# Performance work log

Measured on AMD Instinct MI355X. Metric: run time of the kernel, lower is better.

## Reference

```python
import jax, jax.numpy as jnp
from jax import lax
import numpy as np

HIDDEN = 1024
FEAT = 512
PREV = 10
PRED = 20
BATCH = 1024


def setup_inputs() -> dict:
    key = jax.random.key(0)
    ks = jax.random.split(key, 12)
    s_in = 1.0 / np.sqrt(FEAT)
    s_h = 1.0 / np.sqrt(HIDDEN)
    return {
        "real_input": jax.random.normal(ks[0], (BATCH, PREV + PRED, FEAT), jnp.float32),
        "fake_input": jax.random.normal(ks[1], (BATCH, PRED, FEAT), jnp.float32),
        "Wx": jax.random.normal(ks[2], (FEAT, 4 * HIDDEN), jnp.float32) * s_in,
        "Wh": jax.random.normal(ks[3], (HIDDEN, 4 * HIDDEN), jnp.float32) * s_h,
        "b": jnp.zeros((4 * HIDDEN,), jnp.float32),
        "w2": jax.random.normal(ks[4], (HIDDEN, 1), jnp.float32) * s_h,
        "b2": jnp.zeros((1,), jnp.float32),
        "w3": jax.random.normal(ks[5], (1, 1), jnp.float32),
        "b3": jnp.zeros((1,), jnp.float32),
        "w4": jax.random.normal(ks[6], (1, 1), jnp.float32),
        "b4": jnp.zeros((1,), jnp.float32),
    }


def _lstm_hidden_states(seq, Wx, Wh, b):
    # seq: [B, T, F] -> hidden states hs: [T, B, H]
    B = seq.shape[0]
    xz = jnp.einsum("btf,fk->btk", seq, Wx) + b  # precompute input projections

    def step(carry, xz_t):
        h, c = carry
        z = xz_t + h @ Wh  # [B, 4H]
        i, f, g, o = jnp.split(z, 4, axis=-1)
        i = jax.nn.sigmoid(i)
        f = jax.nn.sigmoid(f)
        g = jnp.tanh(g)
        o = jax.nn.sigmoid(o)
        c = f * c + i * g
        h = o * jnp.tanh(c)
        return (h, c), h

    h0 = jnp.zeros((B, Wh.shape[0]), seq.dtype)
    _, hs = lax.scan(step, (h0, h0), jnp.swapaxes(xz, 0, 1))
    return hs


def _dense_chain(h, w2, b2, w3, b3, w4, b4):
    x = jnp.tanh(h @ w2 + b2)
    x = jnp.tanh(x @ w3 + b3)
    x = jnp.tanh(x @ w4 + b4)
    return x


def reference(real_input, fake_input, Wx, Wh, b, w2, b2, w3, b3, w4, b4):
    # trajectory_real[k] is the prefix real_input[:, :PREV+k+1]; running the
    # LSTM from zero state over each prefix equals taking hidden state at
    # step PREV+k of a single scan over the full sequence.
    fake_seq = jnp.concatenate([real_input[:, :PREV, :], fake_input], axis=1)

    hs_real = _lstm_hidden_states(real_input, Wx, Wh, b)[PREV:PREV + PRED]  # [PRED,B,H]
    hs_fake = _lstm_hidden_states(fake_seq, Wx, Wh, b)[PREV:PREV + PRED]

    real_pred = _dense_chain(hs_real, w2, b2, w3, b3, w4, b4)  # [PRED,B,1]
    fake_pred = _dense_chain(hs_fake, w2, b2, w3, b3, w4, b4)

    real_pred = jnp.swapaxes(real_pred, 0, 1)  # [B,PRED,1]
    fake_pred = jnp.swapaxes(fake_pred, 0, 1)
    return real_pred, fake_pred
```

## Files before the change

kernel.cpp:

```cpp
#include <hip/hip_runtime.h>
#include <hip/hip_bf16.h>
#include <stdint.h>
#include <string.h>

#define HIDDEN 1024
#define FEAT   512
#define PREV   10
#define PRED   20
#define BATCH  1024
#define KTOT   (HIDDEN + FEAT)
#define N4H    4096
#define TSTEPS (PREV + PRED)
#define NBLK   512
#define NTHR   512

typedef __attribute__((ext_vector_type(8))) short short8;
typedef __attribute__((ext_vector_type(4))) float f32x4;
typedef unsigned long long ull;

typedef __attribute__((address_space(3))) unsigned int u32_lds;
typedef const __attribute__((address_space(1))) unsigned int u32_gbl;

__device__ __forceinline__ void async16(void* lds, const void* g) {
  u32_lds* lp = (u32_lds*)(unsigned int)(uintptr_t)lds;
  u32_gbl* gp = (u32_gbl*)(uintptr_t)g;
  __builtin_amdgcn_global_load_lds(gp, lp, 16, 0, 0);
}

__device__ __forceinline__ float sigmoidf_(float x) {
  return 1.0f / (1.0f + __expf(-x));
}
__device__ __forceinline__ float tanhf_(float x) {
  return 1.0f - 2.0f / (1.0f + __expf(2.0f * x));
}

__device__ __forceinline__ ull cload(const void* p) {
  return __hip_atomic_load((const ull*)p, __ATOMIC_RELAXED, __HIP_MEMORY_SCOPE_AGENT);
}
__device__ __forceinline__ void cstore(void* p, ull v) {
  __hip_atomic_store((ull*)p, v, __ATOMIC_RELAXED, __HIP_MEMORY_SCOPE_AGENT);
}

__global__ void pack_w_kernel(const float* __restrict__ Wx, const float* __restrict__ Wh,
                              __hip_bfloat16* __restrict__ WpT) {
  __shared__ float tile[64][65];
  const int k0 = blockIdx.x * 64, n0 = blockIdx.y * 64;
  const int tid = threadIdx.x;
  const float* src = (k0 < HIDDEN) ? (Wh + (size_t)k0 * N4H) : (Wx + (size_t)(k0 - HIDDEN) * N4H);
  {
    const int jl = tid & 15, g = (tid >> 4) & 3, klb = tid >> 6;
#pragma unroll
    for (int it = 0; it < 16; ++it) {
      int kl = klb + it * 4;
      tile[kl][4 * jl + g] = src[(size_t)kl * N4H + g * HIDDEN + (n0 >> 2) + jl];
    }
  }
  __syncthreads();
  {
    const int kl = tid & 63, nlb = tid >> 6;
#pragma unroll
    for (int it = 0; it < 16; ++it) {
      int nl = nlb + it * 4;
      WpT[(size_t)(n0 + nl) * KTOT + k0 + kl] = __float2bfloat16(tile[kl][nl]);
    }
  }
}

__global__ void pack_bias_kernel(const float* __restrict__ b, float* __restrict__ bp) {
  int n = blockIdx.x * 256 + threadIdx.x;
  if (n < N4H) bp[n] = b[(n & 3) * HIDDEN + (n >> 2)];
}

__global__ void cvt_x_kernel(const float* __restrict__ xr, const float* __restrict__ xf,
                             __hip_bfloat16* __restrict__ xrb, __hip_bfloat16* __restrict__ xfb) {
  const int NR4 = BATCH * TSTEPS * FEAT / 4;
  const int NF4 = BATCH * PRED * FEAT / 4;
  int i = blockIdx.x * 256 + threadIdx.x;
  float4 v;
  __hip_bfloat16* dst;
  if (i < NR4) {
    v = ((const float4*)xr)[i];
    dst = xrb + (size_t)i * 4;
  } else {
    int j = i - NR4;
    if (j >= NF4) return;
    v = ((const float4*)xf)[j];
    dst = xfb + (size_t)j * 4;
  }
  dst[0] = __float2bfloat16(v.x);
  dst[1] = __float2bfloat16(v.y);
  dst[2] = __float2bfloat16(v.z);
  dst[3] = __float2bfloat16(v.w);
}

__global__ __launch_bounds__(512, 4)
void lstm_persistent(const __hip_bfloat16* __restrict__ xrb,
                     const __hip_bfloat16* __restrict__ xfb,
                     const __hip_bfloat16* __restrict__ WpT,
                     const float* __restrict__ biasp,
                     const float* __restrict__ w2,
                     __hip_bfloat16* __restrict__ hb0,
                     __hip_bfloat16* __restrict__ hb1,
                     float* __restrict__ cbuf,
                     float* __restrict__ accout,
                     unsigned* __restrict__ bar) {
  __shared__ __align__(16) char smem[40960];
  char* smA = smem;
  char* smB = smem + 8192;

  const int tid = threadIdx.x;
  const int bid = blockIdx.x;
  const int nt = bid & 15, rt = bid >> 4;
  const int n0 = nt * 256;
  const int r0 = rt * 64;
  const int w = tid >> 6, l = tid & 63;
  const int sub = l >> 3;
  const int csrc = (l & 7) ^ sub;
  const int quad = l >> 4, lrow = l & 15;
  const int wm = w & 1, wn = w >> 1;
  const int row_e = tid >> 3, jq = tid & 7;
  unsigned* cnt = bar;
  unsigned* flag = bar + 32;

  const unsigned short* wp_us = (const unsigned short*)WpT;
  float creg[8] = {0.f, 0.f, 0.f, 0.f, 0.f, 0.f, 0.f, 0.f};

#pragma unroll 1
  for (int t = 0; t < TSTEPS; ++t) {
    const unsigned short* hcur = (const unsigned short*)((t & 1) ? hb1 : hb0);
    unsigned short* hnext = (unsigned short*)((t & 1) ? hb0 : hb1);
    const bool active = (t >= PREV) || (rt < 16);

    if (active) {
      if (t == PREV && r0 >= BATCH) {
#pragma unroll
        for (int h2 = 0; h2 < 2; ++h2) {
          size_t base = (size_t)(r0 - BATCH + row_e) * HIDDEN + nt * 64 + h2 * 32 + jq * 4;
          ull d0 = cload(&cbuf[base]);
          ull d1 = cload(&cbuf[base + 2]);
          float2 f0 = *(float2*)&d0, f1 = *(float2*)&d1;
          creg[h2 * 4 + 0] = f0.x;
          creg[h2 * 4 + 1] = f0.y;
          creg[h2 * 4 + 2] = f1.x;
          creg[h2 * 4 + 3] = f1.y;
        }
      }
      const int r0h = (t == PREV && r0 >= BATCH) ? (r0 - BATCH) : r0;

      f32x4 acc[2][4];
#pragma unroll
      for (int a = 0; a < 2; ++a)
#pragma unroll
        for (int b_ = 0; b_ < 4; ++b_) acc[a][b_] = (f32x4){0.f, 0.f, 0.f, 0.f};

#pragma unroll 1
      for (int kt = 0; kt < KTOT / 64; ++kt) {
        const int k0 = kt * 64;
        const unsigned short* bb = wp_us + (size_t)n0 * KTOT + k0;
#pragma unroll
        for (int it = 0; it < 4; ++it)
          async16(smB + (w * 32 + it * 8) * 128,
                  bb + (size_t)(w * 32 + it * 8 + sub) * KTOT + csrc * 8);
        if (k0 < HIDDEN) {
          const unsigned short* ap = hcur + (size_t)(r0h + w * 8 + sub) * HIDDEN + k0 + csrc * 8;
          ull d0 = cload(ap);
          ull d1 = cload(ap + 4);
          ull* lw = (ull*)(smA + (w * 8 + sub) * 128 + (l & 7) * 16);
          lw[0] = d0;
          lw[1] = d1;
        } else {
          const unsigned short* xb;
          size_t xstr;
          if (r0 < BATCH) {
            xb = (const unsigned short*)xrb + ((size_t)r0 * TSTEPS + t) * FEAT + (k0 - HIDDEN);
            xstr = TSTEPS * FEAT;
          } else {
            xb = (const unsigned short*)xfb + ((size_t)(r0 - BATCH) * PRED + (t - PREV)) * FEAT + (k0 - HIDDEN);
            xstr = PRED * FEAT;
          }
          async16(smA + (w * 8) * 128, xb + (size_t)(w * 8 + sub) * xstr + csrc * 8);
        }
        __syncthreads();
#pragma unroll
        for (int kk = 0; kk < 2; ++kk) {
          const int swz = (((kk << 2) + quad) ^ (lrow & 7)) * 16;
          short8 af[2], bf[4];
#pragma unroll
          for (int mi = 0; mi < 2; ++mi)
            af[mi] = *(const short8*)(smA + (wm * 32 + mi * 16 + lrow) * 128 + swz);
#pragma unroll
          for (int ni = 0; ni < 4; ++ni)
            bf[ni] = *(const short8*)(smB + (wn * 64 + ni * 16 + lrow) * 128 + swz);
#pragma unroll
          for (int mi = 0; mi < 2; ++mi)
#pragma unroll
            for (int ni = 0; ni < 4; ++ni)
              acc[mi][ni] = __builtin_amdgcn_mfma_f32_16x16x32_bf16(af[mi], bf[ni], acc[mi][ni], 0, 0, 0);
        }
        __syncthreads();
      }

      float* zb = (float*)smem;
      const int kout = t - PREV;
#pragma unroll 1
      for (int h2 = 0; h2 < 2; ++h2) {
        if ((wn >> 1) == h2) {
          const int cb = (wn & 1) * 64;
#pragma unroll
          for (int mi = 0; mi < 2; ++mi)
#pragma unroll
            for (int ni = 0; ni < 4; ++ni) {
              f32x4 v = acc[mi][ni];
              int col = cb + ni * 16 + lrow;
              int rb = wm * 32 + mi * 16 + quad * 4;
#pragma unroll
              for (int r = 0; r < 4; ++r) zb[(rb + r) * 132 + col] = v[r];
            }
        }
        __syncthreads();
        unsigned short hs[4];
        float cn[4];
        float psum = 0.f;
#pragma unroll
        for (int it = 0; it < 4; ++it) {
          int jloc = jq * 4 + it;
          float4 z4 = *(float4*)&zb[row_e * 132 + jloc * 4];
          float4 bi = *(const float4*)&biasp[n0 + h2 * 128 + jloc * 4];
          int jg = nt * 64 + h2 * 32 + jloc;
          float gi = sigmoidf_(z4.x + bi.x);
          float gf = sigmoidf_(z4.y + bi.y);
          float gg = tanhf_(z4.z + bi.z);
          float go = sigmoidf_(z4.w + bi.w);
          int ci = h2 * 4 + it;
          float cnew = gf * creg[ci] + gi * gg;
          float hnew = go * tanhf_(cnew);
          creg[ci] = cnew;
          cn[it] = cnew;
          __hip_bfloat16 hbv = __float2bfloat16(hnew);
          hs[it] = *(unsigned short*)&hbv;
          if (t >= PREV) psum += hnew * w2[jg];
        }
        const int rg = r0 + row_e;
        const int jg0 = nt * 64 + h2 * 32 + jq * 4;
        ull hpack;
        memcpy(&hpack, hs, 8);
        cstore(&hnext[(size_t)rg * HIDDEN + jg0], hpack);
        if (t == PREV - 1) {
          ull c01, c23;
          memcpy(&c01, &cn[0], 8);
          memcpy(&c23, &cn[2], 8);
          cstore(&cbuf[(size_t)rg * HIDDEN + jg0], c01);
          cstore(&cbuf[(size_t)rg * HIDDEN + jg0 + 2], c23);
        }
        if (t >= PREV) {
          psum += __shfl_down(psum, 4, 8);
          psum += __shfl_down(psum, 2, 8);
          psum += __shfl_down(psum, 1, 8);
          if ((tid & 7) == 0) atomicAdd(&accout[rg * PRED + kout], psum);
        }
        __syncthreads();
      }
    }

    if (t < TSTEPS - 1) {
      __syncthreads();
      if (tid == 0) {
        unsigned ph = (unsigned)(t + 1);
        unsigned old = __hip_atomic_fetch_add(cnt, 1u, __ATOMIC_RELAXED, __HIP_MEMORY_SCOPE_AGENT);
        if (old == NBLK - 1) {
          __hip_atomic_store(cnt, 0u, __ATOMIC_RELAXED, __HIP_MEMORY_SCOPE_AGENT);
          __hip_atomic_store(flag, ph, __ATOMIC_RELAXED, __HIP_MEMORY_SCOPE_AGENT);
        } else {
          while (__hip_atomic_load(flag, __ATOMIC_RELAXED, __HIP_MEMORY_SCOPE_AGENT) < ph)
            __builtin_amdgcn_s_sleep(4);
        }
      }
      __syncthreads();
    }
  }
}

__global__ void final_kernel(const float* __restrict__ accout, const float* __restrict__ b2,
                             const float* __restrict__ w3, const float* __restrict__ b3,
                             const float* __restrict__ w4, const float* __restrict__ b4,
                             float* __restrict__ out) {
  int i = blockIdx.x * 256 + threadIdx.x;
  const int half = BATCH * PRED;
  if (i >= 2 * half) return;
  int r, k;
  if (i < half) {
    r = i / PRED;
    k = i % PRED;
  } else {
    r = BATCH + (i - half) / PRED;
    k = (i - half) % PRED;
  }
  float x = tanhf_(accout[r * PRED + k] + b2[0]);
  x = tanhf_(x * w3[0] + b3[0]);
  x = tanhf_(x * w4[0] + b4[0]);
  out[i] = x;
}

extern "C" void kernel_launch(void* const* d_in, const int* in_sizes, int n_in,
                              void* d_out, int out_size, void* d_ws, size_t ws_size,
                              hipStream_t stream) {
  const float* real_input = (const float*)d_in[0];
  const float* fake_input = (const float*)d_in[1];
  const float* Wx = (const float*)d_in[2];
  const float* Wh = (const float*)d_in[3];
  const float* b  = (const float*)d_in[4];
  const float* w2 = (const float*)d_in[5];
  const float* b2 = (const float*)d_in[6];
  const float* w3 = (const float*)d_in[7];
  const float* b3 = (const float*)d_in[8];
  const float* w4 = (const float*)d_in[9];
  const float* b4 = (const float*)d_in[10];
  float* out = (float*)d_out;

  char* ws = (char*)d_ws;
  size_t off = 0;
  __hip_bfloat16* WpT = (__hip_bfloat16*)(ws + off);  off += (size_t)N4H * KTOT * 2;
  float* biasp = (float*)(ws + off);                  off += (size_t)N4H * 4;
  __hip_bfloat16* xrb = (__hip_bfloat16*)(ws + off);  off += (size_t)BATCH * TSTEPS * FEAT * 2;
  __hip_bfloat16* xfb = (__hip_bfloat16*)(ws + off);  off += (size_t)BATCH * PRED * FEAT * 2;
  __hip_bfloat16* hb0 = (__hip_bfloat16*)(ws + off);  off += (size_t)2 * BATCH * HIDDEN * 2;
  __hip_bfloat16* hb1 = (__hip_bfloat16*)(ws + off);  off += (size_t)2 * BATCH * HIDDEN * 2;
  float* cbuf = (float*)(ws + off);                   off += (size_t)BATCH * HIDDEN * 4;
  float* accout = (float*)(ws + off);                 off += (size_t)2 * BATCH * PRED * 4;
  unsigned* bar = (unsigned*)(ws + off);              off += 256;

  hipMemsetAsync(hb0, 0, (size_t)2 * BATCH * HIDDEN * 2, stream);
  hipMemsetAsync(accout, 0, (size_t)2 * BATCH * PRED * 4, stream);
  hipMemsetAsync(bar, 0, 256, stream);

  pack_w_kernel<<<dim3(KTOT / 64, N4H / 64), 256, 0, stream>>>(Wx, Wh, WpT);
  pack_bias_kernel<<<N4H / 256, 256, 0, stream>>>(b, biasp);
  {
    int n4 = BATCH * TSTEPS * FEAT / 4 + BATCH * PRED * FEAT / 4;
    cvt_x_kernel<<<(n4 + 255) / 256, 256, 0, stream>>>(real_input, fake_input, xrb, xfb);
  }

  {
    const __hip_bfloat16* a_xrb = xrb;
    const __hip_bfloat16* a_xfb = xfb;
    const __hip_bfloat16* a_WpT = WpT;
    const float* a_biasp = biasp;
    const float* a_w2 = w2;
    __hip_bfloat16* a_hb0 = hb0;
    __hip_bfloat16* a_hb1 = hb1;
    float* a_cbuf = cbuf;
    float* a_acc = accout;
    unsigned* a_bar = bar;
    void* args[10] = {&a_xrb, &a_xfb, &a_WpT, &a_biasp, &a_w2,
                      &a_hb0, &a_hb1, &a_cbuf, &a_acc, &a_bar};
    hipError_t e = hipLaunchCooperativeKernel((const void*)lstm_persistent,
                                              dim3(NBLK), dim3(NTHR), args, 0, stream);
    if (e != hipSuccess) {
      lstm_persistent<<<dim3(NBLK), dim3(NTHR), 0, stream>>>(
          xrb, xfb, WpT, biasp, w2, hb0, hb1, cbuf, accout, bar);
    }
  }

  final_kernel<<<(2 * BATCH * PRED + 255) / 256, 256, 0, stream>>>(accout, b2, w3, b3, w4, b4, out);
}
```

Baseline: 1.307 ms.

## Retile LSTM step with double-buffered LDS and phase-specific tile shapes

Splits the per-step GEMM into a templated helper that uses 128-column N tiles (32 tiles) with 64-row M tiles in the shared prefix phase and 128-row M tiles in the two-branch phase, so all 512 blocks stay busy during the first PREV steps instead of half sitting idle. It double-buffers A and B in LDS, prefetching the next K slice (async weight loads, register-staged h loads) while the MFMAs run on the current one. LDS use grows to 64KB per block, which may reduce occupancy, and the extra barriers and changed gate/c-state indexing add complexity.

```diff
diff --git a/kernel.cpp b/kernel.cpp
--- a/kernel.cpp
+++ b/kernel.cpp
@@ -39,6 +39,9 @@
 }
 __device__ __forceinline__ void cstore(void* p, ull v) {
   __hip_atomic_store((ull*)p, v, __ATOMIC_RELAXED, __HIP_MEMORY_SCOPE_AGENT);
+}
+__device__ __forceinline__ void cstore4(void* p, unsigned v) {
+  __hip_atomic_store((unsigned*)p, v, __ATOMIC_RELAXED, __HIP_MEMORY_SCOPE_AGENT);
 }
 
 __global__ void pack_w_kernel(const float* __restrict__ Wx, const float* __restrict__ Wh,
@@ -93,6 +96,179 @@
   dst[3] = __float2bfloat16(v.w);
 }
 
+template <int MT>
+__device__ __forceinline__ void do_step(
+    const unsigned short* __restrict__ hcur, unsigned short* __restrict__ hnext,
+    const unsigned short* __restrict__ xrb, const unsigned short* __restrict__ xfb,
+    const unsigned short* __restrict__ wp_us, const float* __restrict__ biasp,
+    const float* __restrict__ w2, float* __restrict__ cbuf,
+    float* __restrict__ accout, float* __restrict__ creg, char* smem,
+    int t, int r0, int r0a, int nt,
+    int tid, int w, int l, int sub, int csrc, int quad, int lrow) {
+
+  const int n0 = nt * 128;
+  constexpr int NK = KTOT / 64;
+  constexpr int AM = MT / 32;
+  constexpr int AIT = MT / 64;
+  const int wm = w & 1, wn = w >> 1;
+  const int mbase = wm * (MT / 2);
+  const int arow = w * 8 + sub;
+
+  char* sA[2] = {smem, smem + 16384};
+  char* sB[2] = {smem + 32768, smem + 49152};
+
+  f32x4 acc[AM][2];
+#pragma unroll
+  for (int a = 0; a < AM; ++a) {
+    acc[a][0] = (f32x4){0.f, 0.f, 0.f, 0.f};
+    acc[a][1] = (f32x4){0.f, 0.f, 0.f, 0.f};
+  }
+
+  const unsigned short* xbase;
+  size_t xstr;
+  if (r0 < BATCH) {
+    xbase = xrb + ((size_t)r0 * TSTEPS + t) * FEAT;
+    xstr = (size_t)TSTEPS * FEAT;
+  } else {
+    xbase = xfb + ((size_t)(r0 - BATCH) * PRED + (t - PREV)) * FEAT;
+    xstr = (size_t)PRED * FEAT;
+  }
+
+  ull ar[AIT][2];
+
+  {
+    const unsigned short* bb = wp_us + (size_t)n0 * KTOT;
+#pragma unroll
+    for (int it = 0; it < 2; ++it)
+      async16(sB[0] + (it * 64 + w * 8) * 128, bb + (size_t)(it * 64 + arow) * KTOT + csrc * 8);
+#pragma unroll
+    for (int it = 0; it < AIT; ++it) {
+      const unsigned short* ap = hcur + (size_t)(r0a + it * 64 + arow) * HIDDEN + csrc * 8;
+      ar[it][0] = cload(ap);
+      ar[it][1] = cload(ap + 4);
+    }
+  }
+
+#pragma unroll 1
+  for (int kt = 0; kt < NK; ++kt) {
+    const int p = kt & 1, pn = p ^ 1;
+    const int k0 = kt * 64;
+    const bool hk = (k0 < HIDDEN);
+    __syncthreads();
+    if (hk) {
+#pragma unroll
+      for (int it = 0; it < AIT; ++it) {
+        ull* lw = (ull*)(sA[p] + (it * 64 + arow) * 128 + (l & 7) * 16);
+        lw[0] = ar[it][0];
+        lw[1] = ar[it][1];
+      }
+      __syncthreads();
+    }
+    if (kt + 1 < NK) {
+      const int k1 = k0 + 64;
+      const unsigned short* bb = wp_us + (size_t)n0 * KTOT + k1;
+#pragma unroll
+      for (int it = 0; it < 2; ++it)
+        async16(sB[pn] + (it * 64 + w * 8) * 128, bb + (size_t)(it * 64 + arow) * KTOT + csrc * 8);
+      if (k1 < HIDDEN) {
+#pragma unroll
+        for (int it = 0; it < AIT; ++it) {
+          const unsigned short* ap = hcur + (size_t)(r0a + it * 64 + arow) * HIDDEN + k1 + csrc * 8;
+          ar[it][0] = cload(ap);
+          ar[it][1] = cload(ap + 4);
+        }
+      } else {
+#pragma unroll
+        for (int it = 0; it < AIT; ++it)
+          async16(sA[pn] + (it * 64 + w * 8) * 128,
+                  xbase + (size_t)(it * 64 + arow) * xstr + (k1 - HIDDEN) + csrc * 8);
+      }
+    }
+#pragma unroll
+    for (int kk = 0; kk < 2; ++kk) {
+      const int swz = (((kk << 2) + quad) ^ (lrow & 7)) * 16;
+      short8 af[AM], bf[2];
+#pragma unroll
+      for (int mi = 0; mi < AM; ++mi)
+        af[mi] = *(const short8*)(sA[p] + (mbase + mi * 16 + lrow) * 128 + swz);
+#pragma unroll
+      for (int ni = 0; ni < 2; ++ni)
+        bf[ni] = *(const short8*)(sB[p] + (wn * 32 + ni * 16 + lrow) * 128 + swz);
+#pragma unroll
+      for (int mi = 0; mi < AM; ++mi)
+#pragma unroll
+        for (int ni = 0; ni < 2; ++ni)
+          acc[mi][ni] = __builtin_amdgcn_mfma_f32_16x16x32_bf16(af[mi], bf[ni], acc[mi][ni], 0, 0, 0);
+    }
+  }
+  __syncthreads();
+
+  float* zb = (float*)smem;
+  const int kout = t - PREV;
+  constexpr int JT = (MT == 128) ? 4 : 2;
+  const int row_e = (MT == 128) ? (tid >> 2) : (tid >> 3);
+  const int jq = (MT == 128) ? (tid & 3) : (tid & 7);
+#pragma unroll 1
+  for (int h2 = 0; h2 < 2; ++h2) {
+    if ((wn >> 1) == h2) {
+      const int cb = (wn & 1) * 32;
+#pragma unroll
+      for (int mi = 0; mi < AM; ++mi)
+#pragma unroll
+        for (int ni = 0; ni < 2; ++ni) {
+          f32x4 v = acc[mi][ni];
+          const int col = cb + ni * 16 + lrow;
+          const int rb = mbase + mi * 16 + quad * 4;
+#pragma unroll
+          for (int r = 0; r < 4; ++r) zb[(rb + r) * 68 + col] = v[r];
+        }
+    }
+    __syncthreads();
+    unsigned short hs[JT];
+    float cn[JT];
+    float psum = 0.f;
+#pragma unroll
+    for (int it = 0; it < JT; ++it) {
+      const int jloc = jq * JT + it;
+      float4 z4 = *(float4*)&zb[row_e * 68 + jloc * 4];
+      float4 bi = *(const float4*)&biasp[n0 + h2 * 64 + jloc * 4];
+      const int jg = nt * 32 + h2 * 16 + jloc;
+      float gi = sigmoidf_(z4.x + bi.x);
+      float gf = sigmoidf_(z4.y + bi.y);
+      float gg = tanhf_(z4.z + bi.z);
+      float go = sigmoidf_(z4.w + bi.w);
+      const int ci = h2 * JT + it;
+      float cnew = gf * creg[ci] + gi * gg;
+      float hnew = go * tanhf_(cnew);
+      creg[ci] = cnew;
+      cn[it] = cnew;
+      __hip_bfloat16 hbv = __float2bfloat16(hnew);
+      hs[it] = *(unsigned short*)&hbv;
+      if (MT == 128) psum += hnew * w2[jg];
+    }
+    const int rg = r0 + row_e;
+    const int jg0 = nt * 32 + h2 * 16 + jq * JT;
+    if (MT == 128) {
+      ull hp;
+      memcpy(&hp, hs, 8);
+      cstore(&hnext[(size_t)rg * HIDDEN + jg0], hp);
+      psum += __shfl_down(psum, 2, 4);
+      psum += __shfl_down(psum, 1, 4);
+      if ((tid & 3) == 0) atomicAdd(&accout[rg * PRED + kout], psum);
+    } else {
+      unsigned hp;
+      memcpy(&hp, hs, 4);
+      cstore4(&hnext[(size_t)rg * HIDDEN + jg0], hp);
+      if (t == PREV - 1) {
+        ull cp_;
+        memcpy(&cp_, cn, 8);
+        cstore(&cbuf[(size_t)rg * HIDDEN + jg0], cp_);
+      }
+    }
+    __syncthreads();
+  }
+}
+
 __global__ __launch_bounds__(512, 4)
 void lstm_persistent(const __hip_bfloat16* __restrict__ xrb,
                      const __hip_bfloat16* __restrict__ xfb,
@@ -104,21 +280,14 @@
                      float* __restrict__ cbuf,
                      float* __restrict__ accout,
                      unsigned* __restrict__ bar) {
-  __shared__ __align__(16) char smem[40960];
-  char* smA = smem;
-  char* smB = smem + 8192;
-
+  __shared__ __align__(16) char smem[65536];
   const int tid = threadIdx.x;
   const int bid = blockIdx.x;
-  const int nt = bid & 15, rt = bid >> 4;
-  const int n0 = nt * 256;
-  const int r0 = rt * 64;
+  const int nt = bid & 31, rt = bid >> 5;
   const int w = tid >> 6, l = tid & 63;
   const int sub = l >> 3;
   const int csrc = (l & 7) ^ sub;
   const int quad = l >> 4, lrow = l & 15;
-  const int wm = w & 1, wn = w >> 1;
-  const int row_e = tid >> 3, jq = tid & 7;
   unsigned* cnt = bar;
   unsigned* flag = bar + 32;
 
@@ -129,13 +298,20 @@
   for (int t = 0; t < TSTEPS; ++t) {
     const unsigned short* hcur = (const unsigned short*)((t & 1) ? hb1 : hb0);
     unsigned short* hnext = (unsigned short*)((t & 1) ? hb0 : hb1);
-    const bool active = (t >= PREV) || (rt < 16);
-
-    if (active) {
-      if (t == PREV && r0 >= BATCH) {
+
+    if (t < PREV) {
+      const int r0 = rt * 64;
+      do_step<64>(hcur, hnext, (const unsigned short*)xrb, (const unsigned short*)xfb,
+                  wp_us, biasp, w2, cbuf, accout, creg, smem,
+                  t, r0, r0, nt, tid, w, l, sub, csrc, quad, lrow);
+    } else {
+      const int r0 = rt * 128;
+      if (t == PREV) {
+        const int row_e = tid >> 2, jq = tid & 3;
+        const int r0c = (r0 >= BATCH) ? r0 - BATCH : r0;
 #pragma unroll
         for (int h2 = 0; h2 < 2; ++h2) {
-          size_t base = (size_t)(r0 - BATCH + row_e) * HIDDEN + nt * 64 + h2 * 32 + jq * 4;
+          size_t base = (size_t)(r0c + row_e) * HIDDEN + nt * 32 + h2 * 16 + jq * 4;
           ull d0 = cload(&cbuf[base]);
           ull d1 = cload(&cbuf[base + 2]);
           float2 f0 = *(float2*)&d0, f1 = *(float2*)&d1;
@@ -145,121 +321,10 @@
           creg[h2 * 4 + 3] = f1.y;
         }
       }
-      const int r0h = (t == PREV && r0 >= BATCH) ? (r0 - BATCH) : r0;
-
-      f32x4 acc[2][4];
-#pragma unroll
-      for (int a = 0; a < 2; ++a)
-#pragma unroll
-        for (int b_ = 0; b_ < 4; ++b_) acc[a][b_] = (f32x4){0.f, 0.f, 0.f, 0.f};
-
-#pragma unroll 1
-      for (int kt = 0; kt < KTOT / 64; ++kt) {
-        const int k0 = kt * 64;
-        const unsigned short* bb = wp_us + (size_t)n0 * KTOT + k0;
-#pragma unroll
-        for (int it = 0; it < 4; ++it)
-          async16(smB + (w * 32 + it * 8) * 128,
-                  bb + (size_t)(w * 32 + it * 8 + sub) * KTOT + csrc * 8);
-        if (k0 < HIDDEN) {
-          const unsigned short* ap = hcur + (size_t)(r0h + w * 8 + sub) * HIDDEN + k0 + csrc * 8;
-          ull d0 = cload(ap);
-          ull d1 = cload(ap + 4);
-          ull* lw = (ull*)(smA + (w * 8 + sub) * 128 + (l & 7) * 16);
-          lw[0] = d0;
-          lw[1] = d1;
-        } else {
-          const unsigned short* xb;
-          size_t xstr;
-          if (r0 < BATCH) {
-            xb = (const unsigned short*)xrb + ((size_t)r0 * TSTEPS + t) * FEAT + (k0 - HIDDEN);
-            xstr = TSTEPS * FEAT;
-          } else {
-            xb = (const unsigned short*)xfb + ((size_t)(r0 - BATCH) * PRED + (t - PREV)) * FEAT + (k0 - HIDDEN);
-            xstr = PRED * FEAT;
-          }
-          async16(smA + (w * 8) * 128, xb + (size_t)(w * 8 + sub) * xstr + csrc * 8);
-        }
-        __syncthreads();
-#pragma unroll
-        for (int kk = 0; kk < 2; ++kk) {
-          const int swz = (((kk << 2) + quad) ^ (lrow & 7)) * 16;
-          short8 af[2], bf[4];
-#pragma unroll
-          for (int mi = 0; mi < 2; ++mi)
-            af[mi] = *(const short8*)(smA + (wm * 32 + mi * 16 + lrow) * 128 + swz);
-#pragma unroll
-          for (int ni = 0; ni < 4; ++ni)
-            bf[ni] = *(const short8*)(smB + (wn * 64 + ni * 16 + lrow) * 128 + swz);
-#pragma unroll
-          for (int mi = 0; mi < 2; ++mi)
-#pragma unroll
-            for (int ni = 0; ni < 4; ++ni)
-              acc[mi][ni] = __builtin_amdgcn_mfma_f32_16x16x32_bf16(af[mi], bf[ni], acc[mi][ni], 0, 0, 0);
-        }
-        __syncthreads();
-      }
-
-      float* zb = (float*)smem;
-      const int kout = t - PREV;
-#pragma unroll 1
-      for (int h2 = 0; h2 < 2; ++h2) {
-        if ((wn >> 1) == h2) {
-          const int cb = (wn & 1) * 64;
-#pragma unroll
-          for (int mi = 0; mi < 2; ++mi)
-#pragma unroll
-            for (int ni = 0; ni < 4; ++ni) {
-              f32x4 v = acc[mi][ni];
-              int col = cb + ni * 16 + lrow;
-              int rb = wm * 32 + mi * 16 + quad * 4;
-#pragma unroll
-              for (int r = 0; r < 4; ++r) zb[(rb + r) * 132 + col] = v[r];
-            }
-        }
-        __syncthreads();
-        unsigned short hs[4];
-        float cn[4];
-        float psum = 0.f;
-#pragma unroll
-        for (int it = 0; it < 4; ++it) {
-          int jloc = jq * 4 + it;
-          float4 z4 = *(float4*)&zb[row_e * 132 + jloc * 4];
-          float4 bi = *(const float4*)&biasp[n0 + h2 * 128 + jloc * 4];
-          int jg = nt * 64 + h2 * 32 + jloc;
-          float gi = sigmoidf_(z4.x + bi.x);
-          float gf = sigmoidf_(z4.y + bi.y);
-          float gg = tanhf_(z4.z + bi.z);
-          float go = sigmoidf_(z4.w + bi.w);
-          int ci = h2 * 4 + it;
-          float cnew = gf * creg[ci] + gi * gg;
-          float hnew = go * tanhf_(cnew);
-          creg[ci] = cnew;
-          cn[it] = cnew;
-          __hip_bfloat16 hbv = __float2bfloat16(hnew);
-          hs[it] = *(unsigned short*)&hbv;
-          if (t >= PREV) psum += hnew * w2[jg];
-        }
-        const int rg = r0 + row_e;
-        const int jg0 = nt * 64 + h2 * 32 + jq * 4;
-        ull hpack;
-        memcpy(&hpack, hs, 8);
-        cstore(&hnext[(size_t)rg * HIDDEN + jg0], hpack);
-        if (t == PREV - 1) {
-          ull c01, c23;
-          memcpy(&c01, &cn[0], 8);
-          memcpy(&c23, &cn[2], 8);
-          cstore(&cbuf[(size_t)rg * HIDDEN + jg0], c01);
-          cstore(&cbuf[(size_t)rg * HIDDEN + jg0 + 2], c23);
-        }
-        if (t >= PREV) {
-          psum += __shfl_down(psum, 4, 8);
-          psum += __shfl_down(psum, 2, 8);
-          psum += __shfl_down(psum, 1, 8);
-          if ((tid & 7) == 0) atomicAdd(&accout[rg * PRED + kout], psum);
-        }
-        __syncthreads();
-      }
+      const int r0a = (t == PREV && r0 >= BATCH) ? r0 - BATCH : r0;
+      do_step<128>(hcur, hnext, (const unsigned short*)xrb, (const unsigned short*)xfb,
+                   wp_us, biasp, w2, cbuf, accout, creg, smem,
+                   t, r0, r0a, nt, tid, w, l, sub, csrc, quad, lrow);
     }
 
     if (t < TSTEPS - 1) {
```

Measured after the change: 1.927 ms. 47.5% more time.
